# Kernel optimization log

Measured on AMD Instinct MI355X. Metric: run time of the kernel, lower is better.

Reference implementation:

```python
import jax, jax.numpy as jnp
import numpy as np

DIM = 768
N_HEADS = 12
HEAD_DIM = DIM // N_HEADS


def setup_inputs() -> dict:
    key = jax.random.key(0)
    ks = jax.random.split(key, 7)
    B, N = 8, 1024
    s = 1.0 / np.sqrt(DIM)
    return {
        "x": jax.random.normal(ks[0], (B, N, DIM), dtype=jnp.float32),
        "Wq": jax.random.normal(ks[1], (DIM, DIM), dtype=jnp.float32) * s,
        "bq": jnp.zeros((DIM,), dtype=jnp.float32),
        "Wk": jax.random.normal(ks[2], (DIM, DIM), dtype=jnp.float32) * s,
        "bk": jnp.zeros((DIM,), dtype=jnp.float32),
        "Wv": jax.random.normal(ks[3], (DIM, DIM), dtype=jnp.float32) * s,
        "bv": jnp.zeros((DIM,), dtype=jnp.float32),
    }


def _split_heads(t):
    # [b, n, (h d)] -> [b, h, n, d]
    b, n, _ = t.shape
    return t.reshape(b, n, N_HEADS, HEAD_DIM).transpose(0, 2, 1, 3)


def reference(x, Wq, bq, Wk, bk, Wv, bv):
    q = _split_heads(x @ Wq + bq)
    k = _split_heads(x @ Wk + bk)
    v = _split_heads(x @ Wv + bv)
    scores = jnp.einsum('bhqd,bhkd->bhqk', q, k) / np.sqrt(HEAD_DIM).astype(np.float32)
    attn = jax.nn.softmax(scores, axis=-1)
    out = jnp.einsum('bhqk,bhkd->bhqd', attn, v)
    b, h, n, d = out.shape
    return out.transpose(0, 2, 1, 3).reshape(b, n, h * d)
```

## Files before the change

kernel.cpp:

```cpp
#include <hip/hip_runtime.h>

typedef unsigned short u16;
typedef unsigned int u32;
typedef __attribute__((ext_vector_type(8))) short bf16x8;
typedef __attribute__((ext_vector_type(8))) unsigned short u16x8;
typedef __attribute__((ext_vector_type(4))) unsigned short u16x4;
typedef __attribute__((ext_vector_type(4))) float f32x4;

#define GLD_LDS16(g, l)                                                        \
  __builtin_amdgcn_global_load_lds(                                            \
      (const __attribute__((address_space(1))) void*)(g),                      \
      (__attribute__((address_space(3))) void*)(l), 16, 0, 0)
#define VMCNT(n) asm volatile("s_waitcnt vmcnt(" #n ")" ::: "memory")
#define SBAR()                                                                 \
  do {                                                                         \
    __builtin_amdgcn_s_barrier();                                              \
    __builtin_amdgcn_sched_barrier(0);                                         \
  } while (0)

__device__ inline u16 f2b(float f) {
  union { float f; unsigned u; } v; v.f = f;
  unsigned u = v.u + 0x7FFFu + ((v.u >> 16) & 1u);
  return (u16)(u >> 16);
}

__device__ __forceinline__ u32 cvt_pk(float lo, float hi) {
  u32 r;
  asm("v_cvt_pk_bf16_f32 %0, %1, %2" : "=v"(r) : "v"(lo), "v"(hi));
  return r;
}

__global__ __launch_bounds__(256) void k_prep(const float* __restrict__ x,
                                              const float* __restrict__ Wq,
                                              const float* __restrict__ Wk,
                                              const float* __restrict__ Wv,
                                              u16* __restrict__ xb,
                                              u16* __restrict__ Wt) {
  __shared__ u16 T[64][72];
  int tid = threadIdx.x;
  int bid = blockIdx.x;
  if (bid < 3072) {
    size_t i = (size_t)bid * 256 + tid;
    const float* src = x + i * 8;
    f32x4 a = *(const f32x4*)(src);
    f32x4 b = *(const f32x4*)(src + 4);
    u16x8 o;
#pragma unroll
    for (int j = 0; j < 4; j++) { o[j] = f2b(a[j]); o[j + 4] = f2b(b[j]); }
    *(u16x8*)(xb + i * 8) = o;
    return;
  }
  int b2 = bid - 3072;
  int k0 = (b2 % 12) * 64, n0 = ((b2 / 12) % 12) * 64, m = b2 / 144;
  const float* W = (m == 0) ? Wq : ((m == 1) ? Wk : Wv);
#pragma unroll
  for (int i = 0; i < 4; i++) {
    int idx = tid + i * 256;
    int row = idx >> 4, quad = idx & 15;
    f32x4 v = *(const f32x4*)&W[(size_t)(k0 + row) * 768 + n0 + quad * 4];
    u16x4 pk;
#pragma unroll
    for (int j = 0; j < 4; j++) pk[j] = f2b(v[j]);
    *(u16x4*)&T[row][quad * 4] = pk;
  }
  __syncthreads();
#pragma unroll
  for (int i = 0; i < 2; i++) {
    int idx = tid + i * 256;
    int nr = idx >> 3, chunk = idx & 7;
    u16x8 o;
#pragma unroll
    for (int j = 0; j < 8; j++) o[j] = T[chunk * 8 + j][nr];
    *(u16x8*)&Wt[(size_t)m * 589824 + (size_t)(n0 + nr) * 768 + k0 + chunk * 8] = o;
  }
}


#define STAGE(kt, buf)                                                         \
  do {                                                                         \
    _Pragma("unroll") for (int ia_ = 0; ia_ < 2; ++ia_) {                      \
      int od_ = (ia_ * 512 + tid) * 16;                                        \
      int r_ = od_ >> 7;                                                       \
      int c_ = (od_ & 127) ^ ((r_ & 7) << 4);                                  \
      GLD_LDS16(xA + (size_t)r_ * 1536 + (kt) * 128 + c_,                      \
                SB + (buf) * 40960 + od_);                                     \
    }                                                                          \
    _Pragma("unroll") for (int ib_ = 0; ib_ < 3; ++ib_) {                      \
      int od_ = (ib_ * 512 + tid) * 16;                                        \
      int r_ = od_ >> 7;                                                       \
      int c_ = (od_ & 127) ^ ((r_ & 7) << 4);                                  \
      GLD_LDS16(xB + (size_t)r_ * 1536 + (kt) * 128 + c_,                      \
                SB + (buf) * 40960 + 16384 + od_);                             \
    }                                                                          \
  } while (0)

__global__ __launch_bounds__(512, 2) void k_gemm_qkv(
    const u16* __restrict__ xb, const u16* __restrict__ Wt,
    const float* __restrict__ bq, const float* __restrict__ bk,
    const float* __restrict__ bv, u16* __restrict__ Qb, u16* __restrict__ Kb,
    u16* __restrict__ VT) {
  extern __shared__ char SB[];
  int tid = threadIdx.x, w = tid >> 6, lane = tid & 63;
  int lq = lane & 15, g = lane >> 4;
  int wm = w >> 2, wn = w & 3;
  int swz = (lq & 7) << 4;

  int bid = blockIdx.x;
  int sw = (bid & 7) * 96 + (bid >> 3);
  int bm = sw / 12, bn = sw % 12;
  int m0 = bm * 128;
  int z = bn >> 2;
  int nz0 = (bn & 3) * 192;

  const char* xA = (const char*)xb + (size_t)m0 * 1536;
  const char* xB = (const char*)Wt + (size_t)z * 1179648 + (size_t)nz0 * 1536;

  f32x4 acc[4][3];
#pragma unroll
  for (int i = 0; i < 4; i++)
#pragma unroll
    for (int j = 0; j < 3; j++) acc[i][j] = (f32x4){0.f, 0.f, 0.f, 0.f};

  STAGE(0, 0);
  STAGE(1, 1);
  VMCNT(5);
  SBAR();

#pragma unroll
  for (int kt = 0; kt < 12; ++kt) {
    const int cur = kt % 3;
    if (kt < 10) STAGE(kt + 2, (kt + 2) % 3);
    bf16x8 af[4][2], bf[3][2];
#pragma unroll
    for (int mi = 0; mi < 4; ++mi)
#pragma unroll
      for (int kk = 0; kk < 2; ++kk)
        af[mi][kk] = *(const bf16x8*)(SB + cur * 40960 +
                                      (wm * 64 + mi * 16 + lq) * 128 +
                                      ((kk * 64 + g * 16) ^ swz));
#pragma unroll
    for (int nj = 0; nj < 3; ++nj)
#pragma unroll
      for (int kk = 0; kk < 2; ++kk)
        bf[nj][kk] = *(const bf16x8*)(SB + cur * 40960 + 16384 +
                                      (wn * 48 + nj * 16 + lq) * 128 +
                                      ((kk * 64 + g * 16) ^ swz));
    __builtin_amdgcn_s_setprio(1);
#pragma unroll
    for (int mi = 0; mi < 4; ++mi)
#pragma unroll
      for (int nj = 0; nj < 3; ++nj)
#pragma unroll
        for (int kk = 0; kk < 2; ++kk)
          acc[mi][nj] = __builtin_amdgcn_mfma_f32_16x16x32_bf16(
              af[mi][kk], bf[nj][kk], acc[mi][nj], 0, 0, 0);
    __builtin_amdgcn_s_setprio(0);
    if (kt <= 9) {
      VMCNT(5);
      SBAR();
    } else if (kt == 10) {
      VMCNT(0);
      SBAR();
    }
  }

  const float* bias = (z == 0) ? bq : ((z == 1) ? bk : bv);
  if (z < 2) {
    u16* outp = (z == 0) ? Qb : Kb;
    float scale = (z == 0) ? 0.18033688f : 1.0f;
#pragma unroll
    for (int nj = 0; nj < 3; ++nj) {
      int col = nz0 + wn * 48 + nj * 16 + lq;
      float bval = bias[col];
      int h = col >> 6, d = col & 63;
#pragma unroll
      for (int mi = 0; mi < 4; ++mi)
#pragma unroll
        for (int r = 0; r < 4; ++r) {
          int tok = m0 + wm * 64 + mi * 16 + g * 4 + r;
          outp[(((size_t)(tok >> 10) * 12 + h) * 1024 + (tok & 1023)) * 64 +
               d] = f2b((acc[mi][nj][r] + bval) * scale);
        }
    }
  } else {
    __syncthreads();
    u16* T = (u16*)SB;
#pragma unroll
    for (int nj = 0; nj < 3; ++nj) {
      int col = nz0 + wn * 48 + nj * 16 + lq;
      float bval = bias[col];
#pragma unroll
      for (int mi = 0; mi < 4; ++mi) {
        u16x4 pk;
#pragma unroll
        for (int r = 0; r < 4; ++r) pk[r] = f2b(acc[mi][nj][r] + bval);
        *(u16x4*)&T[(wn * 48 + nj * 16 + lq) * 136 + wm * 64 + mi * 16 +
                    g * 4] = pk;
      }
    }
    __syncthreads();
    int bB = m0 >> 10, nn0 = m0 & 1023;
#pragma unroll
    for (int i = 0; i < 6; ++i) {
      int idx = tid + i * 512;
      int row = idx >> 4, ch = idx & 15;
      int col = nz0 + row;
      int h = col >> 6, d = col & 63;
      int base = ((ch >> 3) << 6) | (((ch & 7) >> 2) << 5) | ((ch & 3) << 2);
      u16x4 lo = *(const u16x4*)&T[row * 136 + base];
      u16x4 hi = *(const u16x4*)&T[row * 136 + base + 16];
      u16x8 o8;
      o8[0] = lo[0]; o8[1] = lo[1]; o8[2] = lo[2]; o8[3] = lo[3];
      o8[4] = hi[0]; o8[5] = hi[1]; o8[6] = hi[2]; o8[7] = hi[3];
      *(u16x8*)&VT[((size_t)(bB * 12 + h) * 64 + d) * 1024 + nn0 + ch * 8] = o8;
    }
  }
}

__device__ __forceinline__ void stage_kv(const char* Kg, const char* Vg,
                                         char* SB, int bufoff, int kvi,
                                         int tid) {
#pragma unroll
  for (int it = 0; it < 2; ++it) {
    int od = (tid + it * 256) * 16;
    int ol = od ^ (((od >> 7) & 7) << 4);
    GLD_LDS16(Kg + (size_t)kvi * 8192 + ol, SB + bufoff + od);
    GLD_LDS16(Vg + (size_t)(ol >> 7) * 2048 + kvi * 128 + (ol & 127),
              SB + bufoff + 8192 + od);
  }
}

__global__ __launch_bounds__(256, 3) void k_attn(const u16* __restrict__ Qb,
                                                 const u16* __restrict__ Kb,
                                                 const u16* __restrict__ VT,
                                                 float* __restrict__ out) {
  __shared__ char SB[49152];

  int tid = threadIdx.x, w = tid >> 6, lane = tid & 63;
  int lq = lane & 15, g = lane >> 4;
  int bh = blockIdx.x, qb = blockIdx.y;
  int b = bh / 12, h = bh % 12;
  const u16* Qh = Qb + (size_t)bh * 65536;
  const char* Kg = (const char*)(Kb + (size_t)bh * 65536);
  const char* Vg = (const char*)(VT + (size_t)bh * 65536);
  int q0 = qb * 128 + w * 32;
  int swz = (lane & 7) << 4;

  bf16x8 qf[2][2];
#pragma unroll
  for (int qt = 0; qt < 2; qt++)
#pragma unroll
    for (int kk = 0; kk < 2; kk++)
      qf[qt][kk] = *(const bf16x8*)&Qh[(size_t)(q0 + qt * 16 + lq) * 64 +
                                       kk * 32 + g * 8];

  float m2[2] = {-1e30f, -1e30f}, l2[2] = {0.f, 0.f};
  f32x4 o[2][4];
#pragma unroll
  for (int qt = 0; qt < 2; qt++)
#pragma unroll
    for (int dt = 0; dt < 4; dt++) o[qt][dt] = (f32x4){0.f, 0.f, 0.f, 0.f};

  stage_kv(Kg, Vg, SB, 0, 0, tid);
  stage_kv(Kg, Vg, SB, 16384, 1, tid);

  for (int kv = 0; kv < 16; ++kv) {
    if (kv < 15) {
      VMCNT(4);
    } else {
      VMCNT(0);
    }
    SBAR();
    if (kv <= 13)
      stage_kv(Kg, Vg, SB, ((kv + 2) % 3) * 16384, kv + 2, tid);

    const char* KsB = SB + (kv % 3) * 16384;
    const char* VsB = KsB + 8192;

    f32x4 sa[2][4];
    __builtin_amdgcn_s_setprio(1);
#pragma unroll
    for (int t = 0; t < 4; t++) {
      bf16x8 k0 = *(const bf16x8*)(KsB + (((t * 16 + lq) * 128 + g * 16) ^ swz));
      bf16x8 k1 = *(const bf16x8*)(KsB + (((t * 16 + lq) * 128 + 64 + g * 16) ^ swz));
#pragma unroll
      for (int qt = 0; qt < 2; qt++) {
        sa[qt][t] = __builtin_amdgcn_mfma_f32_16x16x32_bf16(
            k0, qf[qt][0], (f32x4){0.f, 0.f, 0.f, 0.f}, 0, 0, 0);
        sa[qt][t] = __builtin_amdgcn_mfma_f32_16x16x32_bf16(
            k1, qf[qt][1], sa[qt][t], 0, 0, 0);
      }
    }
    __builtin_amdgcn_s_setprio(0);

    bf16x8 pa[2][2];
#pragma unroll
    for (int qt = 0; qt < 2; qt++) {
      float pm = sa[qt][0][0];
#pragma unroll
      for (int t = 0; t < 4; t++)
#pragma unroll
        for (int r = 0; r < 4; r++) pm = fmaxf(pm, sa[qt][t][r]);
      pm = fmaxf(pm, __shfl_xor(pm, 16));
      pm = fmaxf(pm, __shfl_xor(pm, 32));
      if (!__all(pm <= m2[qt] + 8.0f)) {
        float mn = fmaxf(m2[qt], pm);
        float al = __builtin_amdgcn_exp2f(m2[qt] - mn);
        m2[qt] = mn;
        l2[qt] *= al;
        float alr[4];
#pragma unroll
        for (int r = 0; r < 4; r++) alr[r] = __shfl(al, g * 4 + r);
#pragma unroll
        for (int dt = 0; dt < 4; dt++)
#pragma unroll
          for (int r = 0; r < 4; r++) o[qt][dt][r] *= alr[r];
      }
      float ps = 0.f;
#pragma unroll
      for (int t = 0; t < 4; t++)
#pragma unroll
        for (int r = 0; r < 4; r++) {
          float e = __builtin_amdgcn_exp2f(sa[qt][t][r] - m2[qt]);
          sa[qt][t][r] = e;
          ps += e;
        }
      ps += __shfl_xor(ps, 16);
      ps += __shfl_xor(ps, 32);
      l2[qt] += ps;

#pragma unroll
      for (int kk = 0; kk < 2; kk++) {
        u32 w0 = cvt_pk(sa[qt][2 * kk][0], sa[qt][2 * kk][1]);
        u32 w1 = cvt_pk(sa[qt][2 * kk][2], sa[qt][2 * kk][3]);
        u32 w2 = cvt_pk(sa[qt][2 * kk + 1][0], sa[qt][2 * kk + 1][1]);
        u32 w3 = cvt_pk(sa[qt][2 * kk + 1][2], sa[qt][2 * kk + 1][3]);
        union { u32 u[4]; bf16x8 v; } cv;
        cv.u[0] = w0; cv.u[1] = w1; cv.u[2] = w2; cv.u[3] = w3;
        pa[qt][kk] = cv.v;
      }
    }

    __builtin_amdgcn_s_setprio(1);
#pragma unroll
    for (int kk = 0; kk < 2; kk++) {
#pragma unroll
      for (int dt = 0; dt < 4; dt++) {
        bf16x8 vb = *(const bf16x8*)(VsB +
            (((dt * 16 + lq) * 128 + kk * 64 + g * 16) ^ swz));
#pragma unroll
        for (int qt = 0; qt < 2; qt++)
          o[qt][dt] = __builtin_amdgcn_mfma_f32_16x16x32_bf16(pa[qt][kk], vb,
                                                              o[qt][dt], 0, 0, 0);
      }
    }
    __builtin_amdgcn_s_setprio(0);
  }

#pragma unroll
  for (int qt = 0; qt < 2; qt++) {
    float lr[4];
#pragma unroll
    for (int r = 0; r < 4; r++) lr[r] = __shfl(l2[qt], g * 4 + r);
#pragma unroll
    for (int dt = 0; dt < 4; dt++)
#pragma unroll
      for (int r = 0; r < 4; r++) {
        int q = q0 + qt * 16 + g * 4 + r;
        out[((size_t)b * 1024 + q) * 768 + h * 64 + dt * 16 + lq] =
            o[qt][dt][r] / lr[r];
      }
  }
}

extern "C" void kernel_launch(void* const* d_in, const int* in_sizes, int n_in,
                              void* d_out, int out_size, void* d_ws,
                              size_t ws_size, hipStream_t stream) {
  const float* x  = (const float*)d_in[0];
  const float* Wq = (const float*)d_in[1];
  const float* bq = (const float*)d_in[2];
  const float* Wk = (const float*)d_in[3];
  const float* bk = (const float*)d_in[4];
  const float* Wv = (const float*)d_in[5];
  const float* bv = (const float*)d_in[6];
  float* out = (float*)d_out;

  char* ws = (char*)d_ws;
  u16* xb = (u16*)ws;
  u16* Wt = (u16*)(ws + 12582912);
  u16* Qb = (u16*)(ws + 16121856);
  u16* Kb = (u16*)(ws + 28704768);
  u16* VT = (u16*)(ws + 41287680);

  hipFuncSetAttribute((const void*)k_gemm_qkv,
                      hipFuncAttributeMaxDynamicSharedMemorySize, 122880);

  k_prep<<<3504, 256, 0, stream>>>(x, Wq, Wk, Wv, xb, Wt);
  k_gemm_qkv<<<768, 512, 122880, stream>>>(xb, Wt, bq, bk, bv, Qb, Kb, VT);
  k_attn<<<dim3(96, 8), 256, 0, stream>>>(Qb, Kb, VT, out);
}
```

Measured before the change: 171.1 us.

## Compute softmax row sums via MFMA with ones vector and defer max shuffles

Replaces the per-lane exp sum and its cross-lane shuffle reduction with an extra MFMA that multiplies the bf16 probabilities by a ones vector, so the row sums accumulate in the same layout as the output. The max-reduction shuffles now run only when the lazy rescale branch is taken, and the final divide becomes a reciprocal multiply. The kv loop is also fully unrolled. This trims VALU and shuffle work in the softmax in exchange for four extra MFMAs per tile and sums taken from bf16-rounded probabilities. Skipping the cross-lane max when the threshold test passes relies on per-lane maxima, which remains correct because the __all check still covers every lane.

```diff
diff --git a/kernel.cpp b/kernel.cpp
--- a/kernel.cpp
+++ b/kernel.cpp
@@ -254,16 +254,24 @@
       qf[qt][kk] = *(const bf16x8*)&Qh[(size_t)(q0 + qt * 16 + lq) * 64 +
                                        kk * 32 + g * 8];
 
-  float m2[2] = {-1e30f, -1e30f}, l2[2] = {0.f, 0.f};
+  bf16x8 ones8;
+#pragma unroll
+  for (int j = 0; j < 8; j++) ones8[j] = (short)0x3F80;
+
+  float m2[2] = {-1e30f, -1e30f};
+  f32x4 l2a[2];
   f32x4 o[2][4];
 #pragma unroll
-  for (int qt = 0; qt < 2; qt++)
+  for (int qt = 0; qt < 2; qt++) {
+    l2a[qt] = (f32x4){0.f, 0.f, 0.f, 0.f};
 #pragma unroll
     for (int dt = 0; dt < 4; dt++) o[qt][dt] = (f32x4){0.f, 0.f, 0.f, 0.f};
+  }
 
   stage_kv(Kg, Vg, SB, 0, 0, tid);
   stage_kv(Kg, Vg, SB, 16384, 1, tid);
 
+#pragma unroll
   for (int kv = 0; kv < 16; ++kv) {
     if (kv < 15) {
       VMCNT(4);
@@ -301,33 +309,27 @@
       for (int t = 0; t < 4; t++)
 #pragma unroll
         for (int r = 0; r < 4; r++) pm = fmaxf(pm, sa[qt][t][r]);
-      pm = fmaxf(pm, __shfl_xor(pm, 16));
-      pm = fmaxf(pm, __shfl_xor(pm, 32));
       if (!__all(pm <= m2[qt] + 8.0f)) {
+        pm = fmaxf(pm, __shfl_xor(pm, 16));
+        pm = fmaxf(pm, __shfl_xor(pm, 32));
         float mn = fmaxf(m2[qt], pm);
         float al = __builtin_amdgcn_exp2f(m2[qt] - mn);
         m2[qt] = mn;
-        l2[qt] *= al;
         float alr[4];
 #pragma unroll
         for (int r = 0; r < 4; r++) alr[r] = __shfl(al, g * 4 + r);
 #pragma unroll
+        for (int r = 0; r < 4; r++) l2a[qt][r] *= alr[r];
+#pragma unroll
         for (int dt = 0; dt < 4; dt++)
 #pragma unroll
           for (int r = 0; r < 4; r++) o[qt][dt][r] *= alr[r];
       }
-      float ps = 0.f;
 #pragma unroll
       for (int t = 0; t < 4; t++)
 #pragma unroll
-        for (int r = 0; r < 4; r++) {
-          float e = __builtin_amdgcn_exp2f(sa[qt][t][r] - m2[qt]);
-          sa[qt][t][r] = e;
-          ps += e;
-        }
-      ps += __shfl_xor(ps, 16);
-      ps += __shfl_xor(ps, 32);
-      l2[qt] += ps;
+        for (int r = 0; r < 4; r++)
+          sa[qt][t][r] = __builtin_amdgcn_exp2f(sa[qt][t][r] - m2[qt]);
 
 #pragma unroll
       for (int kk = 0; kk < 2; kk++) {
@@ -345,6 +347,10 @@
 #pragma unroll
     for (int kk = 0; kk < 2; kk++) {
 #pragma unroll
+      for (int qt = 0; qt < 2; qt++)
+        l2a[qt] = __builtin_amdgcn_mfma_f32_16x16x32_bf16(pa[qt][kk], ones8,
+                                                          l2a[qt], 0, 0, 0);
+#pragma unroll
       for (int dt = 0; dt < 4; dt++) {
         bf16x8 vb = *(const bf16x8*)(VsB +
             (((dt * 16 + lq) * 128 + kk * 64 + g * 16) ^ swz));
@@ -359,16 +365,16 @@
 
 #pragma unroll
   for (int qt = 0; qt < 2; qt++) {
-    float lr[4];
-#pragma unroll
-    for (int r = 0; r < 4; r++) lr[r] = __shfl(l2[qt], g * 4 + r);
+    float inv[4];
+#pragma unroll
+    for (int r = 0; r < 4; r++) inv[r] = __builtin_amdgcn_rcpf(l2a[qt][r]);
 #pragma unroll
     for (int dt = 0; dt < 4; dt++)
 #pragma unroll
       for (int r = 0; r < 4; r++) {
         int q = q0 + qt * 16 + g * 4 + r;
         out[((size_t)b * 1024 + q) * 768 + h * 64 + dt * 16 + lq] =
-            o[qt][dt][r] / lr[r];
+            o[qt][dt][r] * inv[r];
       }
   }
 }
```

New measurement: 162.6 us. -5.0%, faster.
